# Performance work log

Measured on AMD Instinct MI355X. Metric: run time of the kernel, lower is better.

## Reference

```python
import math
import jax, jax.numpy as jnp
import numpy as np

DIM = 256
B = 32
M = 2048
N = 2048


def setup_inputs() -> dict:
    key = jax.random.key(0)
    k1, k2, k3, k4 = jax.random.split(key, 4)
    query = jax.random.normal(k1, (B, DIM, M), dtype=jnp.float32)
    key_t = jax.random.normal(k2, (B, DIM, N), dtype=jnp.float32)
    value = jax.random.normal(k3, (B, DIM, N), dtype=jnp.float32)
    # orthogonal random projection via QR, as in the torch __init__
    proj = np.asarray(jax.random.normal(k4, (DIM, DIM), dtype=jnp.float32))
    orth_proj, _ = np.linalg.qr(proj)
    orth_proj = jnp.asarray(orth_proj, dtype=jnp.float32)
    return {"query": query, "key": key_t, "value": value, "orth_proj": orth_proj}


def reference(query, key, value, orth_proj):
    dim = orth_proj.shape[0]
    q = query / math.sqrt(dim)
    # kernel feature maps: relu(W^T x), channels-first layout b c m
    phi_q = jax.nn.relu(jnp.einsum('bcm,ce->bem', q, orth_proj))
    phi_k = jax.nn.relu(jnp.einsum('bcn,ce->ben', key, orth_proj))
    phi_k_rowsum = phi_k.sum(-1)                         # [b, e]
    scale = jnp.einsum('bem,be->bm', phi_q, phi_k_rowsum)  # [b, m]
    scale = 1.0 / (scale + 1e-8)
    phi_q = phi_q * scale[:, None, :]                    # [b, e, m]
    kv = jnp.einsum('ben,bdn->bed', phi_k, value)        # [b, e, d]
    out = jnp.einsum('bem,bed->bdm', phi_q, kv)          # [b, d, m]
    return out
```

## Files before the change

### kernel.cpp

```cpp
#include <hip/hip_runtime.h>

#define DIMC 256
#define BSZ  32
#define MDIM 2048
#define NDIM 2048

typedef __attribute__((ext_vector_type(8))) short bf16x8;
typedef __attribute__((ext_vector_type(4))) float f32x4;

static __device__ __forceinline__ unsigned short f2bf(float x) {
  unsigned int u = __float_as_uint(x);
  u += 0x7fffu + ((u >> 16) & 1u);
  return (unsigned short)(u >> 16);
}
static __device__ __forceinline__ float bf2f(unsigned short h) {
  return __uint_as_float(((unsigned int)h) << 16);
}

static __device__ __forceinline__ void gl_lds16(const void* g, void* l) {
  __builtin_amdgcn_global_load_lds(
      (const __attribute__((address_space(1))) unsigned int*)g,
      (__attribute__((address_space(3))) unsigned int*)l, 16, 0, 0);
}

__global__ __launch_bounds__(256) void wt_kernel(
    const float* __restrict__ W, unsigned short* __restrict__ Wt) {
  const int e = blockIdx.x, c = threadIdx.x;
  Wt[e * 256 + c] = f2bf(W[c * 256 + e]);
}

__global__ __launch_bounds__(256) void vconv_kernel(
    const float* __restrict__ v, unsigned short* __restrict__ vb) {
  const size_t i = ((size_t)blockIdx.x * 256 + threadIdx.x) * 8;
  float4 a = *(const float4*)(v + i);
  float4 b = *(const float4*)(v + i + 4);
  unsigned short t[8] __attribute__((aligned(16)));
  t[0] = f2bf(a.x); t[1] = f2bf(a.y); t[2] = f2bf(a.z); t[3] = f2bf(a.w);
  t[4] = f2bf(b.x); t[5] = f2bf(b.y); t[6] = f2bf(b.z); t[7] = f2bf(b.w);
  *(uint4*)(vb + i) = *(const uint4*)t;
}

__global__ __launch_bounds__(256) void phiq_kernel(
    const float* __restrict__ X, const unsigned short* __restrict__ Wt,
    unsigned short* __restrict__ phi) {
  __shared__ unsigned short As[128 * 32];
  __shared__ unsigned short Bs[128 * 40];
  const int b = blockIdx.z;
  const int m0 = blockIdx.x * 128;
  const int e0 = blockIdx.y * 128;
  const int t = threadIdx.x;
  const int lane = t & 63, wave = t >> 6;
  const int wr = wave >> 1, wc = wave & 1;
  const int q = lane >> 4, l15 = lane & 15;
  const float* Xb = X + (size_t)b * DIMC * MDIM;
  const int a1row = t >> 2, a1k = (t & 3) << 3;
  const int midx = t & 127, ch = (t >> 7) << 4;
  f32x4 acc[4][4];
#pragma unroll
  for (int i = 0; i < 4; ++i)
#pragma unroll
    for (int j = 0; j < 4; ++j) acc[i][j] = (f32x4){0.f, 0.f, 0.f, 0.f};

  for (int k0 = 0; k0 < DIMC; k0 += 32) {
    __syncthreads();
    gl_lds16(Wt + (size_t)(e0 + a1row) * DIMC + k0 + a1k, &As[wave * 512]);
    gl_lds16(Wt + (size_t)(e0 + a1row + 64) * DIMC + k0 + a1k,
             &As[2048 + wave * 512]);
    {
      const float* src = Xb + (size_t)(k0 + ch) * MDIM + m0 + midx;
      unsigned short tmp[16] __attribute__((aligned(16)));
#pragma unroll
      for (int i = 0; i < 16; ++i) tmp[i] = f2bf(src[(size_t)i * MDIM]);
      *(uint4*)&Bs[midx * 40 + ch] = *(const uint4*)&tmp[0];
      *(uint4*)&Bs[midx * 40 + ch + 8] = *(const uint4*)&tmp[8];
    }
    __syncthreads();
    bf16x8 a[4], bv[4];
#pragma unroll
    for (int i = 0; i < 4; ++i)
      a[i] = *(const bf16x8*)&As[(wr * 64 + i * 16 + l15) * 32 + q * 8];
#pragma unroll
    for (int j = 0; j < 4; ++j)
      bv[j] = *(const bf16x8*)&Bs[(wc * 64 + j * 16 + l15) * 40 + q * 8];
#pragma unroll
    for (int i = 0; i < 4; ++i)
#pragma unroll
      for (int j = 0; j < 4; ++j)
        acc[i][j] =
            __builtin_amdgcn_mfma_f32_16x16x32_bf16(a[i], bv[j], acc[i][j], 0, 0, 0);
  }
  unsigned short* dst = phi + (size_t)b * MDIM * DIMC;
#pragma unroll
  for (int i = 0; i < 4; ++i)
#pragma unroll
    for (int j = 0; j < 4; ++j) {
      const int m = m0 + wc * 64 + j * 16 + l15;
#pragma unroll
      for (int r = 0; r < 4; ++r) {
        const int e = e0 + wr * 64 + i * 16 + q * 4 + r;
        float v = acc[i][j][r];
        v = v > 0.f ? v * 0.0625f : 0.f;
        dst[(size_t)m * DIMC + e] = f2bf(v);
      }
    }
}

__global__ __launch_bounds__(256) void phik_kernel(
    const float* __restrict__ X, const unsigned short* __restrict__ Wt,
    unsigned short* __restrict__ phi) {
  __shared__ unsigned short As[128 * 32];
  __shared__ unsigned short Bs[128 * 40];
  const int b = blockIdx.z;
  const int n0 = blockIdx.x * 128;
  const int e0 = blockIdx.y * 128;
  const int t = threadIdx.x;
  const int lane = t & 63, wave = t >> 6;
  const int wr = wave >> 1, wc = wave & 1;
  const int q = lane >> 4, l15 = lane & 15;
  const float* Xb = X + (size_t)b * DIMC * NDIM;
  const int a1row = t >> 2, a1k = (t & 3) << 3;
  const int nidx = t & 127, ch = (t >> 7) << 4;
  f32x4 acc[4][4];
#pragma unroll
  for (int i = 0; i < 4; ++i)
#pragma unroll
    for (int j = 0; j < 4; ++j) acc[i][j] = (f32x4){0.f, 0.f, 0.f, 0.f};

  for (int k0 = 0; k0 < DIMC; k0 += 32) {
    __syncthreads();
    gl_lds16(Wt + (size_t)(e0 + a1row) * DIMC + k0 + a1k, &As[wave * 512]);
    gl_lds16(Wt + (size_t)(e0 + a1row + 64) * DIMC + k0 + a1k,
             &As[2048 + wave * 512]);
    {
      const float* src = Xb + (size_t)(k0 + ch) * NDIM + n0 + nidx;
      unsigned short tmp[16] __attribute__((aligned(16)));
#pragma unroll
      for (int i = 0; i < 16; ++i) tmp[i] = f2bf(src[(size_t)i * NDIM]);
      *(uint4*)&Bs[nidx * 40 + ch] = *(const uint4*)&tmp[0];
      *(uint4*)&Bs[nidx * 40 + ch + 8] = *(const uint4*)&tmp[8];
    }
    __syncthreads();
    bf16x8 a[4], bv[4];
#pragma unroll
    for (int i = 0; i < 4; ++i)
      a[i] = *(const bf16x8*)&As[(wr * 64 + i * 16 + l15) * 32 + q * 8];
#pragma unroll
    for (int j = 0; j < 4; ++j)
      bv[j] = *(const bf16x8*)&Bs[(wc * 64 + j * 16 + l15) * 40 + q * 8];
#pragma unroll
    for (int i = 0; i < 4; ++i)
#pragma unroll
      for (int j = 0; j < 4; ++j)
        acc[i][j] =
            __builtin_amdgcn_mfma_f32_16x16x32_bf16(a[i], bv[j], acc[i][j], 0, 0, 0);
  }
  unsigned short* dst = phi + (size_t)b * DIMC * NDIM;
#pragma unroll
  for (int i = 0; i < 4; ++i)
#pragma unroll
    for (int j = 0; j < 4; ++j) {
      const int n = n0 + wc * 64 + j * 16 + l15;
#pragma unroll
      for (int r = 0; r < 4; ++r) {
        const int e = e0 + wr * 64 + i * 16 + q * 4 + r;
        float v = acc[i][j][r];
        dst[(size_t)e * NDIM + n] = f2bf(v > 0.f ? v : 0.f);
      }
    }
}

__global__ __launch_bounds__(256) void rowsum_kernel(
    const unsigned short* __restrict__ phi_k, float* __restrict__ rowsum) {
  const int row = blockIdx.x;
  const unsigned short* p = phi_k + (size_t)row * NDIM;
  uint4 v = *(const uint4*)(p + threadIdx.x * 8);
  const unsigned short* u = (const unsigned short*)&v;
  float s = 0.f;
#pragma unroll
  for (int i = 0; i < 8; ++i) s += bf2f(u[i]);
  __shared__ float red[256];
  red[threadIdx.x] = s;
  __syncthreads();
  for (int w = 128; w >= 1; w >>= 1) {
    if (threadIdx.x < w) red[threadIdx.x] += red[threadIdx.x + w];
    __syncthreads();
  }
  if (threadIdx.x == 0) rowsum[row] = red[0];
}

__global__ __launch_bounds__(256) void kv_kernel(
    const unsigned short* __restrict__ vb,
    const unsigned short* __restrict__ phi_k, float* __restrict__ kv_acc) {
  __shared__ unsigned short As[128 * 32];
  __shared__ unsigned short Bs[128 * 32];
  const int z = blockIdx.z;
  const int b = z >> 2, slice = z & 3;
  const int d0 = blockIdx.x * 128, e0 = blockIdx.y * 128;
  const int t = threadIdx.x;
  const int lane = t & 63, wave = t >> 6;
  const int wr = wave >> 1, wc = wave & 1;
  const int q = lane >> 4, l15 = lane & 15;
  const unsigned short* Ab = vb + (size_t)b * DIMC * NDIM;
  const unsigned short* Bb = phi_k + (size_t)b * DIMC * NDIM;
  const int a1row = t >> 2, a1k = (t & 3) << 3;
  f32x4 acc[4][4];
#pragma unroll
  for (int i = 0; i < 4; ++i)
#pragma unroll
    for (int j = 0; j < 4; ++j) acc[i][j] = (f32x4){0.f, 0.f, 0.f, 0.f};

  const int nbeg = slice * 512;
  for (int n0 = nbeg; n0 < nbeg + 512; n0 += 32) {
    __syncthreads();
    gl_lds16(Ab + (size_t)(d0 + a1row) * NDIM + n0 + a1k, &As[wave * 512]);
    gl_lds16(Ab + (size_t)(d0 + a1row + 64) * NDIM + n0 + a1k,
             &As[2048 + wave * 512]);
    gl_lds16(Bb + (size_t)(e0 + a1row) * NDIM + n0 + a1k, &Bs[wave * 512]);
    gl_lds16(Bb + (size_t)(e0 + a1row + 64) * NDIM + n0 + a1k,
             &Bs[2048 + wave * 512]);
    __syncthreads();
    bf16x8 a[4], bv[4];
#pragma unroll
    for (int i = 0; i < 4; ++i)
      a[i] = *(const bf16x8*)&As[(wr * 64 + i * 16 + l15) * 32 + q * 8];
#pragma unroll
    for (int j = 0; j < 4; ++j)
      bv[j] = *(const bf16x8*)&Bs[(wc * 64 + j * 16 + l15) * 32 + q * 8];
#pragma unroll
    for (int i = 0; i < 4; ++i)
#pragma unroll
      for (int j = 0; j < 4; ++j)
        acc[i][j] =
            __builtin_amdgcn_mfma_f32_16x16x32_bf16(a[i], bv[j], acc[i][j], 0, 0, 0);
  }
  float* kva = kv_acc + (size_t)b * DIMC * DIMC;
#pragma unroll
  for (int i = 0; i < 4; ++i)
#pragma unroll
    for (int j = 0; j < 4; ++j) {
      const int e = e0 + wc * 64 + j * 16 + l15;
#pragma unroll
      for (int r = 0; r < 4; ++r) {
        const int d = d0 + wr * 64 + i * 16 + q * 4 + r;
        atomicAdd(&kva[(size_t)d * DIMC + e], acc[i][j][r]);
      }
    }
}

__global__ __launch_bounds__(256) void kvcvt_kernel(
    const float* __restrict__ acc, unsigned short* __restrict__ kvt) {
  const size_t i = ((size_t)blockIdx.x * 256 + threadIdx.x) * 4;
  float4 a = *(const float4*)(acc + i);
  unsigned short t[4] __attribute__((aligned(8)));
  t[0] = f2bf(a.x); t[1] = f2bf(a.y); t[2] = f2bf(a.z); t[3] = f2bf(a.w);
  *(uint2*)(kvt + i) = *(const uint2*)t;
}

__global__ __launch_bounds__(256) void scale_kernel(
    const unsigned short* __restrict__ phi_q, const float* __restrict__ rowsum,
    float* __restrict__ scale) {
  const int gw = blockIdx.x * 4 + (threadIdx.x >> 6);
  const int b = gw >> 11, m = gw & 2047;
  const int lane = threadIdx.x & 63;
  const unsigned short* p = phi_q + ((size_t)b * MDIM + m) * DIMC + lane * 4;
  uint2 v = *(const uint2*)p;
  const unsigned short* u = (const unsigned short*)&v;
  float4 r = *(const float4*)(rowsum + b * DIMC + lane * 4);
  float s = bf2f(u[0]) * r.x + bf2f(u[1]) * r.y + bf2f(u[2]) * r.z +
            bf2f(u[3]) * r.w;
#pragma unroll
  for (int off = 32; off >= 1; off >>= 1) s += __shfl_down(s, off, 64);
  if (lane == 0) scale[(size_t)b * MDIM + m] = 1.f / (s + 1e-8f);
}

__global__ __launch_bounds__(256) void out_kernel(
    const unsigned short* __restrict__ kv_t,
    const unsigned short* __restrict__ phi_q, const float* __restrict__ scale,
    float* __restrict__ out) {
  __shared__ unsigned short As[128 * 32];
  __shared__ unsigned short Bs[128 * 32];
  const int b = blockIdx.z;
  const int m0 = blockIdx.x * 128;
  const int d0 = blockIdx.y * 128;
  const int t = threadIdx.x;
  const int lane = t & 63, wave = t >> 6;
  const int wr = wave >> 1, wc = wave & 1;
  const int q = lane >> 4, l15 = lane & 15;
  const unsigned short* Ab = kv_t + (size_t)b * DIMC * DIMC;
  const unsigned short* Bb = phi_q + (size_t)b * MDIM * DIMC;
  const int a1row = t >> 2, a1k = (t & 3) << 3;
  f32x4 acc[4][4];
#pragma unroll
  for (int i = 0; i < 4; ++i)
#pragma unroll
    for (int j = 0; j < 4; ++j) acc[i][j] = (f32x4){0.f, 0.f, 0.f, 0.f};

  for (int k0 = 0; k0 < DIMC; k0 += 32) {
    __syncthreads();
    gl_lds16(Ab + (size_t)(d0 + a1row) * DIMC + k0 + a1k, &As[wave * 512]);
    gl_lds16(Ab + (size_t)(d0 + a1row + 64) * DIMC + k0 + a1k,
             &As[2048 + wave * 512]);
    gl_lds16(Bb + (size_t)(m0 + a1row) * DIMC + k0 + a1k, &Bs[wave * 512]);
    gl_lds16(Bb + (size_t)(m0 + a1row + 64) * DIMC + k0 + a1k,
             &Bs[2048 + wave * 512]);
    __syncthreads();
    bf16x8 a[4], bv[4];
#pragma unroll
    for (int i = 0; i < 4; ++i)
      a[i] = *(const bf16x8*)&As[(wr * 64 + i * 16 + l15) * 32 + q * 8];
#pragma unroll
    for (int j = 0; j < 4; ++j)
      bv[j] = *(const bf16x8*)&Bs[(wc * 64 + j * 16 + l15) * 32 + q * 8];
#pragma unroll
    for (int i = 0; i < 4; ++i)
#pragma unroll
      for (int j = 0; j < 4; ++j)
        acc[i][j] =
            __builtin_amdgcn_mfma_f32_16x16x32_bf16(a[i], bv[j], acc[i][j], 0, 0, 0);
  }
  float* ob = out + (size_t)b * DIMC * MDIM;
  const float* scb = scale + (size_t)b * MDIM;
#pragma unroll
  for (int j = 0; j < 4; ++j) {
    const int m = m0 + wc * 64 + j * 16 + l15;
    const float sc = scb[m];
#pragma unroll
    for (int i = 0; i < 4; ++i) {
#pragma unroll
      for (int r = 0; r < 4; ++r) {
        const int d = d0 + wr * 64 + i * 16 + q * 4 + r;
        ob[(size_t)d * MDIM + m] = acc[i][j][r] * sc;
      }
    }
  }
}

extern "C" void kernel_launch(void* const* d_in, const int* in_sizes, int n_in,
                              void* d_out, int out_size, void* d_ws, size_t ws_size,
                              hipStream_t stream) {
  const float* query = (const float*)d_in[0];
  const float* key   = (const float*)d_in[1];
  const float* value = (const float*)d_in[2];
  const float* W     = (const float*)d_in[3];
  float* out = (float*)d_out;

  unsigned short* Wt    = (unsigned short*)d_ws;
  unsigned short* v_bf  = Wt + 65536;
  unsigned short* phi_q = v_bf + (size_t)BSZ * DIMC * NDIM;
  unsigned short* phi_k = phi_q + (size_t)BSZ * MDIM * DIMC;
  unsigned short* kv_t  = phi_k + (size_t)BSZ * DIMC * NDIM;
  float* kv_acc = (float*)(kv_t + (size_t)BSZ * DIMC * DIMC);
  float* rowsum = kv_acc + (size_t)BSZ * DIMC * DIMC;
  float* scale  = rowsum + BSZ * DIMC;

  hipMemsetAsync(kv_acc, 0, (size_t)BSZ * DIMC * DIMC * sizeof(float), stream);
  hipLaunchKernelGGL(wt_kernel, dim3(256), dim3(256), 0, stream, W, Wt);
  hipLaunchKernelGGL(vconv_kernel, dim3(8192), dim3(256), 0, stream, value, v_bf);
  hipLaunchKernelGGL(phiq_kernel, dim3(MDIM / 128, DIMC / 128, BSZ), dim3(256),
                     0, stream, query, Wt, phi_q);
  hipLaunchKernelGGL(phik_kernel, dim3(NDIM / 128, DIMC / 128, BSZ), dim3(256),
                     0, stream, key, Wt, phi_k);
  hipLaunchKernelGGL(rowsum_kernel, dim3(BSZ * DIMC), dim3(256), 0, stream,
                     phi_k, rowsum);
  hipLaunchKernelGGL(kv_kernel, dim3(2, 2, BSZ * 4), dim3(256), 0, stream,
                     v_bf, phi_k, kv_acc);
  hipLaunchKernelGGL(kvcvt_kernel, dim3(2048), dim3(256), 0, stream, kv_acc,
                     kv_t);
  hipLaunchKernelGGL(scale_kernel, dim3(BSZ * MDIM / 4), dim3(256), 0, stream,
                     phi_q, rowsum, scale);
  hipLaunchKernelGGL(out_kernel, dim3(MDIM / 128, DIMC / 128, BSZ), dim3(256),
                     0, stream, kv_t, phi_q, scale, out);
}
```

Measured before the change: 332.7 us.

## Pre-transpose Q/K to bf16, fuse rowsum and scale into phi GEMM epilogues

Adds a tiled transpose kernel that converts query and key to bf16 in [m][c] layout, so the phi GEMMs can load both operands with direct global-to-LDS loads instead of strided per-element fp32 loads. The rowsum is fused into the phi_k epilogue and the scale dot product into the phi_q epilogue, both using shuffle reductions and atomics. This removes the separate rowsum and scale kernels. The value-to-bf16 conversion is folded into kv_kernel, which now uses 8 n-slices, and the reciprocal moves into the out epilogue. In exchange there is an extra transpose pass over Q and K, atomic contention on the reduction buffers, and kv_acc now reuses the tq buffer.

```diff
diff --git a/kernel.cpp b/kernel.cpp
--- a/kernel.cpp
+++ b/kernel.cpp
@@ -29,22 +29,111 @@
   Wt[e * 256 + c] = f2bf(W[c * 256 + e]);
 }
 
-__global__ __launch_bounds__(256) void vconv_kernel(
-    const float* __restrict__ v, unsigned short* __restrict__ vb) {
-  const size_t i = ((size_t)blockIdx.x * 256 + threadIdx.x) * 8;
-  float4 a = *(const float4*)(v + i);
-  float4 b = *(const float4*)(v + i + 4);
-  unsigned short t[8] __attribute__((aligned(16)));
-  t[0] = f2bf(a.x); t[1] = f2bf(a.y); t[2] = f2bf(a.z); t[3] = f2bf(a.w);
-  t[4] = f2bf(b.x); t[5] = f2bf(b.y); t[6] = f2bf(b.z); t[7] = f2bf(b.w);
-  *(uint4*)(vb + i) = *(const uint4*)t;
+__global__ __launch_bounds__(256) void trans_kernel(
+    const float* __restrict__ query, const float* __restrict__ key,
+    unsigned short* __restrict__ tq, unsigned short* __restrict__ tk) {
+  const int z = blockIdx.z;
+  const int b = z & 31;
+  const bool isq = z < 32;
+  const float* in = (isq ? query : key) + (size_t)b * DIMC * MDIM;
+  unsigned short* out = (isq ? tq : tk) + (size_t)b * MDIM * DIMC;
+  const float alpha = isq ? 0.0625f : 1.0f;
+  const int m0 = blockIdx.x * 64, c0 = blockIdx.y * 64;
+  __shared__ float s[64][65];
+  const int t = threadIdx.x;
+  const int r16 = t >> 4, o4 = (t & 15) << 2;
+#pragma unroll
+  for (int p = 0; p < 4; ++p) {
+    const int cl = p * 16 + r16;
+    float4 v = *(const float4*)(in + (size_t)(c0 + cl) * MDIM + m0 + o4);
+    s[cl][o4 + 0] = v.x; s[cl][o4 + 1] = v.y;
+    s[cl][o4 + 2] = v.z; s[cl][o4 + 3] = v.w;
+  }
+  __syncthreads();
+#pragma unroll
+  for (int p = 0; p < 4; ++p) {
+    const int ml = p * 16 + r16;
+    unsigned short o[4] __attribute__((aligned(8)));
+#pragma unroll
+    for (int i = 0; i < 4; ++i) o[i] = f2bf(s[o4 + i][ml] * alpha);
+    *(uint2*)(out + (size_t)(m0 + ml) * DIMC + c0 + o4) = *(const uint2*)o;
+  }
+}
+
+__global__ __launch_bounds__(256) void phik_kernel(
+    const unsigned short* __restrict__ Wt, const unsigned short* __restrict__ tk,
+    unsigned short* __restrict__ phi_k, float* __restrict__ rowsum) {
+  __shared__ unsigned short As[128 * 32];
+  __shared__ unsigned short Bs[128 * 32];
+  const int b = blockIdx.z;
+  const int n0 = blockIdx.x * 128;
+  const int e0 = blockIdx.y * 128;
+  const int t = threadIdx.x;
+  const int lane = t & 63, wave = t >> 6;
+  const int wr = wave >> 1, wc = wave & 1;
+  const int q = lane >> 4, l15 = lane & 15;
+  const unsigned short* Bb = tk + (size_t)b * NDIM * DIMC;
+  const int a1row = t >> 2, a1k = (t & 3) << 3;
+  f32x4 acc[4][4];
+#pragma unroll
+  for (int i = 0; i < 4; ++i)
+#pragma unroll
+    for (int j = 0; j < 4; ++j) acc[i][j] = (f32x4){0.f, 0.f, 0.f, 0.f};
+
+  for (int k0 = 0; k0 < DIMC; k0 += 32) {
+    __syncthreads();
+    gl_lds16(Wt + (size_t)(e0 + a1row) * DIMC + k0 + a1k, &As[wave * 512]);
+    gl_lds16(Wt + (size_t)(e0 + a1row + 64) * DIMC + k0 + a1k,
+             &As[2048 + wave * 512]);
+    gl_lds16(Bb + (size_t)(n0 + a1row) * DIMC + k0 + a1k, &Bs[wave * 512]);
+    gl_lds16(Bb + (size_t)(n0 + a1row + 64) * DIMC + k0 + a1k,
+             &Bs[2048 + wave * 512]);
+    __syncthreads();
+    bf16x8 a[4], bv[4];
+#pragma unroll
+    for (int i = 0; i < 4; ++i)
+      a[i] = *(const bf16x8*)&As[(wr * 64 + i * 16 + l15) * 32 + q * 8];
+#pragma unroll
+    for (int j = 0; j < 4; ++j)
+      bv[j] = *(const bf16x8*)&Bs[(wc * 64 + j * 16 + l15) * 32 + q * 8];
+#pragma unroll
+    for (int i = 0; i < 4; ++i)
+#pragma unroll
+      for (int j = 0; j < 4; ++j)
+        acc[i][j] =
+            __builtin_amdgcn_mfma_f32_16x16x32_bf16(a[i], bv[j], acc[i][j], 0, 0, 0);
+  }
+  unsigned short* dst = phi_k + (size_t)b * DIMC * NDIM;
+#pragma unroll
+  for (int i = 0; i < 4; ++i) {
+#pragma unroll
+    for (int r = 0; r < 4; ++r) {
+      const int e = e0 + wr * 64 + i * 16 + q * 4 + r;
+      float sp = 0.f;
+#pragma unroll
+      for (int j = 0; j < 4; ++j) {
+        const int n = n0 + wc * 64 + j * 16 + l15;
+        float v = acc[i][j][r];
+        v = v > 0.f ? v : 0.f;
+        sp += v;
+        dst[(size_t)e * NDIM + n] = f2bf(v);
+      }
+      sp += __shfl_xor(sp, 1, 64);
+      sp += __shfl_xor(sp, 2, 64);
+      sp += __shfl_xor(sp, 4, 64);
+      sp += __shfl_xor(sp, 8, 64);
+      if (l15 == 0) atomicAdd(&rowsum[b * DIMC + e], sp);
+    }
+  }
 }
 
 __global__ __launch_bounds__(256) void phiq_kernel(
-    const float* __restrict__ X, const unsigned short* __restrict__ Wt,
-    unsigned short* __restrict__ phi) {
+    const unsigned short* __restrict__ tq, const unsigned short* __restrict__ Wt,
+    const float* __restrict__ rowsum, unsigned short* __restrict__ phi_q,
+    float* __restrict__ scale_acc) {
   __shared__ unsigned short As[128 * 32];
-  __shared__ unsigned short Bs[128 * 40];
+  __shared__ unsigned short Bs[128 * 32];
+  __shared__ float rsL[128];
   const int b = blockIdx.z;
   const int m0 = blockIdx.x * 128;
   const int e0 = blockIdx.y * 128;
@@ -52,9 +141,9 @@
   const int lane = t & 63, wave = t >> 6;
   const int wr = wave >> 1, wc = wave & 1;
   const int q = lane >> 4, l15 = lane & 15;
-  const float* Xb = X + (size_t)b * DIMC * MDIM;
+  const unsigned short* Ab = tq + (size_t)b * MDIM * DIMC;
   const int a1row = t >> 2, a1k = (t & 3) << 3;
-  const int midx = t & 127, ch = (t >> 7) << 4;
+  if (t < 128) rsL[t] = rowsum[b * DIMC + e0 + t];
   f32x4 acc[4][4];
 #pragma unroll
   for (int i = 0; i < 4; ++i)
@@ -63,17 +152,12 @@
 
   for (int k0 = 0; k0 < DIMC; k0 += 32) {
     __syncthreads();
-    gl_lds16(Wt + (size_t)(e0 + a1row) * DIMC + k0 + a1k, &As[wave * 512]);
+    gl_lds16(Ab + (size_t)(m0 + a1row) * DIMC + k0 + a1k, &As[wave * 512]);
+    gl_lds16(Ab + (size_t)(m0 + a1row + 64) * DIMC + k0 + a1k,
+             &As[2048 + wave * 512]);
+    gl_lds16(Wt + (size_t)(e0 + a1row) * DIMC + k0 + a1k, &Bs[wave * 512]);
     gl_lds16(Wt + (size_t)(e0 + a1row + 64) * DIMC + k0 + a1k,
-             &As[2048 + wave * 512]);
-    {
-      const float* src = Xb + (size_t)(k0 + ch) * MDIM + m0 + midx;
-      unsigned short tmp[16] __attribute__((aligned(16)));
-#pragma unroll
-      for (int i = 0; i < 16; ++i) tmp[i] = f2bf(src[(size_t)i * MDIM]);
-      *(uint4*)&Bs[midx * 40 + ch] = *(const uint4*)&tmp[0];
-      *(uint4*)&Bs[midx * 40 + ch + 8] = *(const uint4*)&tmp[8];
-    }
+             &Bs[2048 + wave * 512]);
     __syncthreads();
     bf16x8 a[4], bv[4];
 #pragma unroll
@@ -81,7 +165,7 @@
       a[i] = *(const bf16x8*)&As[(wr * 64 + i * 16 + l15) * 32 + q * 8];
 #pragma unroll
     for (int j = 0; j < 4; ++j)
-      bv[j] = *(const bf16x8*)&Bs[(wc * 64 + j * 16 + l15) * 40 + q * 8];
+      bv[j] = *(const bf16x8*)&Bs[(wc * 64 + j * 16 + l15) * 32 + q * 8];
 #pragma unroll
     for (int i = 0; i < 4; ++i)
 #pragma unroll
@@ -89,132 +173,69 @@
         acc[i][j] =
             __builtin_amdgcn_mfma_f32_16x16x32_bf16(a[i], bv[j], acc[i][j], 0, 0, 0);
   }
-  unsigned short* dst = phi + (size_t)b * MDIM * DIMC;
-#pragma unroll
-  for (int i = 0; i < 4; ++i)
-#pragma unroll
-    for (int j = 0; j < 4; ++j) {
-      const int m = m0 + wc * 64 + j * 16 + l15;
-#pragma unroll
-      for (int r = 0; r < 4; ++r) {
-        const int e = e0 + wr * 64 + i * 16 + q * 4 + r;
+  unsigned short* dst = phi_q + (size_t)b * MDIM * DIMC;
+#pragma unroll
+  for (int i = 0; i < 4; ++i) {
+#pragma unroll
+    for (int r = 0; r < 4; ++r) {
+      const int m = m0 + wr * 64 + i * 16 + q * 4 + r;
+      float sp = 0.f;
+#pragma unroll
+      for (int j = 0; j < 4; ++j) {
+        const int e = e0 + wc * 64 + j * 16 + l15;
         float v = acc[i][j][r];
-        v = v > 0.f ? v * 0.0625f : 0.f;
+        v = v > 0.f ? v : 0.f;
+        sp += v * rsL[wc * 64 + j * 16 + l15];
         dst[(size_t)m * DIMC + e] = f2bf(v);
       }
-    }
-}
-
-__global__ __launch_bounds__(256) void phik_kernel(
-    const float* __restrict__ X, const unsigned short* __restrict__ Wt,
-    unsigned short* __restrict__ phi) {
-  __shared__ unsigned short As[128 * 32];
-  __shared__ unsigned short Bs[128 * 40];
-  const int b = blockIdx.z;
-  const int n0 = blockIdx.x * 128;
-  const int e0 = blockIdx.y * 128;
+      sp += __shfl_xor(sp, 1, 64);
+      sp += __shfl_xor(sp, 2, 64);
+      sp += __shfl_xor(sp, 4, 64);
+      sp += __shfl_xor(sp, 8, 64);
+      if (l15 == 0) atomicAdd(&scale_acc[(size_t)b * MDIM + m], sp);
+    }
+  }
+}
+
+__global__ __launch_bounds__(256) void kv_kernel(
+    const float* __restrict__ value, const unsigned short* __restrict__ phi_k,
+    float* __restrict__ kv_acc) {
+  __shared__ unsigned short As[128 * 40];
+  __shared__ unsigned short Bs[128 * 32];
+  const int z = blockIdx.z;
+  const int b = z >> 3, slice = z & 7;
+  const int d0 = blockIdx.x * 128, e0 = blockIdx.y * 128;
   const int t = threadIdx.x;
   const int lane = t & 63, wave = t >> 6;
   const int wr = wave >> 1, wc = wave & 1;
   const int q = lane >> 4, l15 = lane & 15;
-  const float* Xb = X + (size_t)b * DIMC * NDIM;
-  const int a1row = t >> 2, a1k = (t & 3) << 3;
-  const int nidx = t & 127, ch = (t >> 7) << 4;
-  f32x4 acc[4][4];
-#pragma unroll
-  for (int i = 0; i < 4; ++i)
-#pragma unroll
-    for (int j = 0; j < 4; ++j) acc[i][j] = (f32x4){0.f, 0.f, 0.f, 0.f};
-
-  for (int k0 = 0; k0 < DIMC; k0 += 32) {
-    __syncthreads();
-    gl_lds16(Wt + (size_t)(e0 + a1row) * DIMC + k0 + a1k, &As[wave * 512]);
-    gl_lds16(Wt + (size_t)(e0 + a1row + 64) * DIMC + k0 + a1k,
-             &As[2048 + wave * 512]);
-    {
-      const float* src = Xb + (size_t)(k0 + ch) * NDIM + n0 + nidx;
-      unsigned short tmp[16] __attribute__((aligned(16)));
-#pragma unroll
-      for (int i = 0; i < 16; ++i) tmp[i] = f2bf(src[(size_t)i * NDIM]);
-      *(uint4*)&Bs[nidx * 40 + ch] = *(const uint4*)&tmp[0];
-      *(uint4*)&Bs[nidx * 40 + ch + 8] = *(const uint4*)&tmp[8];
-    }
-    __syncthreads();
-    bf16x8 a[4], bv[4];
-#pragma unroll
-    for (int i = 0; i < 4; ++i)
-      a[i] = *(const bf16x8*)&As[(wr * 64 + i * 16 + l15) * 32 + q * 8];
-#pragma unroll
-    for (int j = 0; j < 4; ++j)
-      bv[j] = *(const bf16x8*)&Bs[(wc * 64 + j * 16 + l15) * 40 + q * 8];
-#pragma unroll
-    for (int i = 0; i < 4; ++i)
-#pragma unroll
-      for (int j = 0; j < 4; ++j)
-        acc[i][j] =
-            __builtin_amdgcn_mfma_f32_16x16x32_bf16(a[i], bv[j], acc[i][j], 0, 0, 0);
-  }
-  unsigned short* dst = phi + (size_t)b * DIMC * NDIM;
-#pragma unroll
-  for (int i = 0; i < 4; ++i)
-#pragma unroll
-    for (int j = 0; j < 4; ++j) {
-      const int n = n0 + wc * 64 + j * 16 + l15;
-#pragma unroll
-      for (int r = 0; r < 4; ++r) {
-        const int e = e0 + wr * 64 + i * 16 + q * 4 + r;
-        float v = acc[i][j][r];
-        dst[(size_t)e * NDIM + n] = f2bf(v > 0.f ? v : 0.f);
-      }
-    }
-}
-
-__global__ __launch_bounds__(256) void rowsum_kernel(
-    const unsigned short* __restrict__ phi_k, float* __restrict__ rowsum) {
-  const int row = blockIdx.x;
-  const unsigned short* p = phi_k + (size_t)row * NDIM;
-  uint4 v = *(const uint4*)(p + threadIdx.x * 8);
-  const unsigned short* u = (const unsigned short*)&v;
-  float s = 0.f;
-#pragma unroll
-  for (int i = 0; i < 8; ++i) s += bf2f(u[i]);
-  __shared__ float red[256];
-  red[threadIdx.x] = s;
-  __syncthreads();
-  for (int w = 128; w >= 1; w >>= 1) {
-    if (threadIdx.x < w) red[threadIdx.x] += red[threadIdx.x + w];
-    __syncthreads();
-  }
-  if (threadIdx.x == 0) rowsum[row] = red[0];
-}
-
-__global__ __launch_bounds__(256) void kv_kernel(
-    const unsigned short* __restrict__ vb,
-    const unsigned short* __restrict__ phi_k, float* __restrict__ kv_acc) {
-  __shared__ unsigned short As[128 * 32];
-  __shared__ unsigned short Bs[128 * 32];
-  const int z = blockIdx.z;
-  const int b = z >> 2, slice = z & 3;
-  const int d0 = blockIdx.x * 128, e0 = blockIdx.y * 128;
-  const int t = threadIdx.x;
-  const int lane = t & 63, wave = t >> 6;
-  const int wr = wave >> 1, wc = wave & 1;
-  const int q = lane >> 4, l15 = lane & 15;
-  const unsigned short* Ab = vb + (size_t)b * DIMC * NDIM;
+  const float* Ab = value + (size_t)b * DIMC * NDIM;
   const unsigned short* Bb = phi_k + (size_t)b * DIMC * NDIM;
   const int a1row = t >> 2, a1k = (t & 3) << 3;
+  const int dl = t >> 1, nh = (t & 1) << 4;
   f32x4 acc[4][4];
 #pragma unroll
   for (int i = 0; i < 4; ++i)
 #pragma unroll
     for (int j = 0; j < 4; ++j) acc[i][j] = (f32x4){0.f, 0.f, 0.f, 0.f};
 
-  const int nbeg = slice * 512;
-  for (int n0 = nbeg; n0 < nbeg + 512; n0 += 32) {
-    __syncthreads();
-    gl_lds16(Ab + (size_t)(d0 + a1row) * NDIM + n0 + a1k, &As[wave * 512]);
-    gl_lds16(Ab + (size_t)(d0 + a1row + 64) * NDIM + n0 + a1k,
-             &As[2048 + wave * 512]);
+  const int nbeg = slice * 256;
+  for (int n0 = nbeg; n0 < nbeg + 256; n0 += 32) {
+    __syncthreads();
+    {
+      const float* src = Ab + (size_t)(d0 + dl) * NDIM + n0 + nh;
+      float4 f0 = *(const float4*)(src + 0);
+      float4 f1 = *(const float4*)(src + 4);
+      float4 f2 = *(const float4*)(src + 8);
+      float4 f3 = *(const float4*)(src + 12);
+      unsigned short tmp[16] __attribute__((aligned(16)));
+      tmp[0] = f2bf(f0.x); tmp[1] = f2bf(f0.y); tmp[2] = f2bf(f0.z); tmp[3] = f2bf(f0.w);
+      tmp[4] = f2bf(f1.x); tmp[5] = f2bf(f1.y); tmp[6] = f2bf(f1.z); tmp[7] = f2bf(f1.w);
+      tmp[8] = f2bf(f2.x); tmp[9] = f2bf(f2.y); tmp[10] = f2bf(f2.z); tmp[11] = f2bf(f2.w);
+      tmp[12] = f2bf(f3.x); tmp[13] = f2bf(f3.y); tmp[14] = f2bf(f3.z); tmp[15] = f2bf(f3.w);
+      *(uint4*)&As[dl * 40 + nh] = *(const uint4*)&tmp[0];
+      *(uint4*)&As[dl * 40 + nh + 8] = *(const uint4*)&tmp[8];
+    }
     gl_lds16(Bb + (size_t)(e0 + a1row) * NDIM + n0 + a1k, &Bs[wave * 512]);
     gl_lds16(Bb + (size_t)(e0 + a1row + 64) * NDIM + n0 + a1k,
              &Bs[2048 + wave * 512]);
@@ -222,7 +243,7 @@
     bf16x8 a[4], bv[4];
 #pragma unroll
     for (int i = 0; i < 4; ++i)
-      a[i] = *(const bf16x8*)&As[(wr * 64 + i * 16 + l15) * 32 + q * 8];
+      a[i] = *(const bf16x8*)&As[(wr * 64 + i * 16 + l15) * 40 + q * 8];
 #pragma unroll
     for (int j = 0; j < 4; ++j)
       bv[j] = *(const bf16x8*)&Bs[(wc * 64 + j * 16 + l15) * 32 + q * 8];
@@ -256,27 +277,10 @@
   *(uint2*)(kvt + i) = *(const uint2*)t;
 }
 
-__global__ __launch_bounds__(256) void scale_kernel(
-    const unsigned short* __restrict__ phi_q, const float* __restrict__ rowsum,
-    float* __restrict__ scale) {
-  const int gw = blockIdx.x * 4 + (threadIdx.x >> 6);
-  const int b = gw >> 11, m = gw & 2047;
-  const int lane = threadIdx.x & 63;
-  const unsigned short* p = phi_q + ((size_t)b * MDIM + m) * DIMC + lane * 4;
-  uint2 v = *(const uint2*)p;
-  const unsigned short* u = (const unsigned short*)&v;
-  float4 r = *(const float4*)(rowsum + b * DIMC + lane * 4);
-  float s = bf2f(u[0]) * r.x + bf2f(u[1]) * r.y + bf2f(u[2]) * r.z +
-            bf2f(u[3]) * r.w;
-#pragma unroll
-  for (int off = 32; off >= 1; off >>= 1) s += __shfl_down(s, off, 64);
-  if (lane == 0) scale[(size_t)b * MDIM + m] = 1.f / (s + 1e-8f);
-}
-
 __global__ __launch_bounds__(256) void out_kernel(
     const unsigned short* __restrict__ kv_t,
-    const unsigned short* __restrict__ phi_q, const float* __restrict__ scale,
-    float* __restrict__ out) {
+    const unsigned short* __restrict__ phi_q,
+    const float* __restrict__ scale_acc, float* __restrict__ out) {
   __shared__ unsigned short As[128 * 32];
   __shared__ unsigned short Bs[128 * 32];
   const int b = blockIdx.z;
@@ -319,11 +323,11 @@
             __builtin_amdgcn_mfma_f32_16x16x32_bf16(a[i], bv[j], acc[i][j], 0, 0, 0);
   }
   float* ob = out + (size_t)b * DIMC * MDIM;
-  const float* scb = scale + (size_t)b * MDIM;
+  const float* scb = scale_acc + (size_t)b * MDIM;
 #pragma unroll
   for (int j = 0; j < 4; ++j) {
     const int m = m0 + wc * 64 + j * 16 + l15;
-    const float sc = scb[m];
+    const float sc = 1.f / (scb[m] + 1e-8f);
 #pragma unroll
     for (int i = 0; i < 4; ++i) {
 #pragma unroll
@@ -345,29 +349,29 @@
   float* out = (float*)d_out;
 
   unsigned short* Wt    = (unsigned short*)d_ws;
-  unsigned short* v_bf  = Wt + 65536;
-  unsigned short* phi_q = v_bf + (size_t)BSZ * DIMC * NDIM;
+  unsigned short* tq    = Wt + 65536;
+  unsigned short* tk    = tq + (size_t)BSZ * MDIM * DIMC;
+  unsigned short* phi_q = tk + (size_t)BSZ * NDIM * DIMC;
   unsigned short* phi_k = phi_q + (size_t)BSZ * MDIM * DIMC;
   unsigned short* kv_t  = phi_k + (size_t)BSZ * DIMC * NDIM;
-  float* kv_acc = (float*)(kv_t + (size_t)BSZ * DIMC * DIMC);
-  float* rowsum = kv_acc + (size_t)BSZ * DIMC * DIMC;
-  float* scale  = rowsum + BSZ * DIMC;
-
+  float* rowsum    = (float*)(kv_t + (size_t)BSZ * DIMC * DIMC);
+  float* scale_acc = rowsum + BSZ * DIMC;
+  float* kv_acc    = (float*)tq;
+
+  hipMemsetAsync(rowsum, 0, (size_t)(BSZ * DIMC + BSZ * MDIM) * sizeof(float),
+                 stream);
+  hipLaunchKernelGGL(wt_kernel, dim3(256), dim3(256), 0, stream, W, Wt);
+  hipLaunchKernelGGL(trans_kernel, dim3(MDIM / 64, DIMC / 64, 64), dim3(256),
+                     0, stream, query, key, tq, tk);
+  hipLaunchKernelGGL(phik_kernel, dim3(NDIM / 128, DIMC / 128, BSZ), dim3(256),
+                     0, stream, Wt, tk, phi_k, rowsum);
+  hipLaunchKernelGGL(phiq_kernel, dim3(MDIM / 128, DIMC / 128, BSZ), dim3(256),
+                     0, stream, tq, Wt, rowsum, phi_q, scale_acc);
   hipMemsetAsync(kv_acc, 0, (size_t)BSZ * DIMC * DIMC * sizeof(float), stream);
-  hipLaunchKernelGGL(wt_kernel, dim3(256), dim3(256), 0, stream, W, Wt);
-  hipLaunchKernelGGL(vconv_kernel, dim3(8192), dim3(256), 0, stream, value, v_bf);
-  hipLaunchKernelGGL(phiq_kernel, dim3(MDIM / 128, DIMC / 128, BSZ), dim3(256),
-                     0, stream, query, Wt, phi_q);
-  hipLaunchKernelGGL(phik_kernel, dim3(NDIM / 128, DIMC / 128, BSZ), dim3(256),
-                     0, stream, key, Wt, phi_k);
-  hipLaunchKernelGGL(rowsum_kernel, dim3(BSZ * DIMC), dim3(256), 0, stream,
-                     phi_k, rowsum);
-  hipLaunchKernelGGL(kv_kernel, dim3(2, 2, BSZ * 4), dim3(256), 0, stream,
-                     v_bf, phi_k, kv_acc);
+  hipLaunchKernelGGL(kv_kernel, dim3(2, 2, BSZ * 8), dim3(256), 0, stream,
+                     value, phi_k, kv_acc);
   hipLaunchKernelGGL(kvcvt_kernel, dim3(2048), dim3(256), 0, stream, kv_acc,
                      kv_t);
-  hipLaunchKernelGGL(scale_kernel, dim3(BSZ * MDIM / 4), dim3(256), 0, stream,
-                     phi_q, rowsum, scale);
   hipLaunchKernelGGL(out_kernel, dim3(MDIM / 128, DIMC / 128, BSZ), dim3(256),
-                     0, stream, kv_t, phi_q, scale, out);
-}
+                     0, stream, kv_t, phi_q, scale_acc, out);
+}
```

Result: slower. 355.0 us (+6.7%).
